# Optimization experiments

Measured on AMD Instinct MI355X. Metric: run time of the kernel, lower is better.

The kernel has to match this reference:

```python
import jax, jax.numpy as jnp
import numpy as np
from jax.scipy.linalg import solve_triangular

LS = 0.5414            # frozen GP length scale (_gp_scale.data = 0.5414)
L2 = LS * LS
D = 2
K_OPS = D + 2          # operators: identity, d/dx_i (i=1..d), laplacian
JITTER_KXX = 1e-5
JITTER_AKA = 1e-4
JITTER_YY = 1e-5


def _opiK(xout, xin, l2, d):
    # op_i applied to first arg of RBF kernel -> (bs, k, m, n)
    r = xout[:, :, None, :] - xin[:, None, :, :]            # (bs,m,n,d)
    u = jnp.sum(r * r, axis=-1) / l2                        # (bs,m,n)
    K = jnp.exp(-0.5 * u)
    ri = jnp.moveaxis(r, -1, 1)                             # (bs,d,m,n)
    grad = -(ri / l2) * K[:, None]                          # d/dx_i K
    lap = ((u - d) / l2) * K                                # Lap_x K
    return jnp.concatenate([K[:, None], grad, lap[:, None]], axis=1)


def _opiKopjfull(x, l2, d):
    # op_i on first arg, op_j on second arg -> (bs, k, k, m, m)
    r = x[:, :, None, :] - x[:, None, :, :]
    u = jnp.sum(r * r, axis=-1) / l2
    K = jnp.exp(-0.5 * u)
    ri = jnp.moveaxis(r, -1, 1)                             # (bs,d,m,m)
    gK = (ri / l2) * K[:, None]                             # d/dy_j K
    lapK = ((u - d) / l2) * K                               # Lap K (either arg)
    eye = jnp.eye(d, dtype=x.dtype)[None, :, :, None, None]
    gg = (eye / l2 - ri[:, :, None] * ri[:, None] / (l2 * l2)) * K[:, None, None]  # d/dx_i d/dy_j K
    glap = (ri / (l2 * l2)) * (((2.0 + d - u) * K)[:, None])  # d/dx_i Lap_y K
    laplap = (((u - d) ** 2 - 4.0 * u + 2.0 * d) / (l2 * l2)) * K  # Lap_x Lap_y K
    row0 = jnp.concatenate([K[:, None, None], gK[:, None], lapK[:, None, None]], axis=2)
    rowg = jnp.concatenate([(-gK)[:, :, None], gg, glap[:, :, None]], axis=2)
    rowl = jnp.concatenate([lapK[:, None, None], (-glap)[:, None], laplap[:, None, None]], axis=2)
    return jnp.concatenate([row0, rowg, rowl], axis=1)


def _psd_solve(L, B):
    # (Kxx + jitter I)^{-1} B via Cholesky (stands in for gpytorch inv_matmul/CG)
    y = solve_triangular(L, B, lower=True)
    return solve_triangular(L, y, lower=True, trans=1)


def _forward(xin, meanin, Kin, weight, bias):
    bs, n, c = meanin.shape
    d, k, l2 = D, K_OPS, L2
    xout, m = xin, n
    r = xin[:, :, None, :] - xin[:, None, :, :]
    Kxx = jnp.exp(-0.5 * jnp.sum(r * r, axis=-1) / l2)      # (bs,n,n)
    In = jnp.eye(n, dtype=xin.dtype)
    Lc = jnp.linalg.cholesky(Kxx + JITTER_KXX * In)
    opiKmn = _opiK(xout, xin, l2, d)                        # (bs,k,m,n)
    # posterior mean of op_i applied to the GP
    opimean = (opiKmn.reshape(bs, k * m, n) @ _psd_solve(Lc, meanin)).reshape(bs, k, m, c)
    Amean = jnp.transpose(opimean, (0, 2, 3, 1)).reshape(bs, m, c * k) @ weight.T + bias
    W = weight.reshape(-1, c, k)                            # (cout,c,k)
    W2 = jnp.einsum('oci,ocj->ij', W, W) / W.shape[0]       # (k,k)
    Kxxinvopi = jnp.swapaxes(
        _psd_solve(Lc, jnp.swapaxes(opiKmn.reshape(bs, k * m, n), 1, 2)), 1, 2)  # (bs,km,n)
    interp_weights = jnp.swapaxes(_psd_solve(Lc, Kin), 1, 2)                      # (bs,n,n)
    opi_interp = jnp.transpose((Kxxinvopi @ interp_weights).reshape(bs, k, m, n), (0, 2, 3, 1))  # (bs,m,n,k)
    Ak_interp = (opi_interp @ W2).reshape(bs, m, n * k)
    Im = jnp.eye(m, dtype=xin.dtype)
    AkinA = Ak_interp @ jnp.transpose(opiKmn, (0, 3, 1, 2)).reshape(bs, n * k, m) + JITTER_AKA * Im
    opiKxxxopj = jnp.transpose(
        (Kxxinvopi @ jnp.swapaxes(opiKmn.reshape(bs, k * m, n), 1, 2)).reshape(bs, k, m, k, m),
        (0, 1, 3, 2, 4))                                    # (bs,k,k,m,m)
    ijkyy = _opiKopjfull(xout, l2, d) - opiKxxxopj          # posterior cov of op_i f, op_j f
    AkAyy = jnp.einsum('bijmp,ij->bmp', ijkyy, W2) + JITTER_YY * Im
    full_AKA = AkinA + AkAyy
    return (xout, Amean, full_AKA)


def setup_inputs() -> dict:
    bs, n, cin, cout = 4, 576, 32, 64
    key = jax.random.key(0)
    k1, k2, k3, k4, k5 = jax.random.split(key, 5)
    xin = jax.random.uniform(k1, (bs, n, D), dtype=jnp.float32) * 6.0
    meanin = jax.random.normal(k2, (bs, n, cin), dtype=jnp.float32)
    A = jax.random.normal(k3, (bs, n, n), dtype=jnp.float32) / np.float32(np.sqrt(n))
    Kin = A @ jnp.swapaxes(A, 1, 2) + 0.1 * jnp.eye(n, dtype=jnp.float32)  # PSD covariance
    fan_in = cin * K_OPS
    weight = jax.random.normal(k4, (cout, fan_in), dtype=jnp.float32) / np.float32(np.sqrt(fan_in))
    bias = jax.random.normal(k5, (cout,), dtype=jnp.float32) * 0.01
    return {"xin": xin, "meanin": meanin, "Kin": Kin, "weight": weight, "bias": bias}


def reference(xin, meanin, Kin, weight, bias):
    return _forward(xin, meanin, Kin, weight, bias)
```

## Files before the change

kernel.cpp:

```cpp
#include <hip/hip_runtime.h>
#include <math.h>

#define NPTS 576
#define N2 331776
#define BSZ 4
#define NB 64
#define NT 9

#define INVL2 (1.0f/0.29311396f)

typedef __attribute__((ext_vector_type(8))) short short8v;
typedef __attribute__((ext_vector_type(16))) float f32x16;

__global__ void copy_xout(const float* __restrict__ xin, float* __restrict__ out) {
    int idx = blockIdx.x * 256 + threadIdx.x;
    out[idx] = xin[idx];
}

__global__ void build_k(const float* __restrict__ xin,
                        float* __restrict__ Kxx, float* __restrict__ opiK) {
    int idx = blockIdx.x * 256 + threadIdx.x;
    int b = idx / N2;
    int rem = idx - b * N2;
    int m = rem / NPTS;
    int nn = rem - m * NPTS;
    const float* xb = xin + (size_t)b * NPTS * 2;
    float xm0 = xb[m*2],  xm1 = xb[m*2+1];
    float xn0 = xb[nn*2], xn1 = xb[nn*2+1];
    float r0 = xm0 - xn0, r1 = xm1 - xn1;
    float u = (r0*r0 + r1*r1) * INVL2;
    float Kv = expf(-0.5f * u);
    Kxx[idx] = Kv + ((m == nn) ? 1e-5f : 0.0f);
    size_t base = (size_t)b * 4 * N2 + rem;
    opiK[base]          = Kv;
    opiK[base + N2]     = -r0 * INVL2 * Kv;
    opiK[base + 2*N2]   = -r1 * INVL2 * Kv;
    opiK[base + 3*N2]   = (u - 2.0f) * INVL2 * Kv;
}

__global__ void w2_k(const float* __restrict__ w, float* __restrict__ W2) {
    __shared__ float red[256];
    int tid = threadIdx.x;
    int pair = tid & 15;
    int slice = tid >> 4;
    int i = pair >> 2, j = pair & 3;
    float s = 0.0f;
    for (int o = slice * 4; o < slice * 4 + 4; ++o)
        for (int c = 0; c < 32; ++c)
            s += w[o*128 + c*4 + i] * w[o*128 + c*4 + j];
    red[tid] = s;
    __syncthreads();
    if (tid < 16) {
        float t = 0.0f;
        #pragma unroll
        for (int k = 0; k < 16; ++k) t += red[pair + 16*k];
        W2[pair] = t * (1.0f/64.0f);
    }
}

__device__ void factor_invert_64(float (*T)[NB+1], float (*V)[NB+1],
                                 float (*tmp)[17], int tid) {
    for (int p = 0; p < 4; ++p) {
        int cp = p * 16;
        if (tid < 64) {
            int r = tid;
            float reg[16];
            #pragma unroll
            for (int q = 0; q < 16; ++q) reg[q] = T[r][cp + q];
            #pragma unroll
            for (int j = 0; j < 16; ++j) {
                int col = cp + j;
                float d2 = __shfl(reg[j], col);
                float d = sqrtf(fmaxf(d2, 1e-12f));
                float lr = (r == col) ? d : reg[j] / d;
                reg[j] = lr;
                #pragma unroll
                for (int q = j + 1; q < 16; ++q) {
                    float lc = __shfl(lr, cp + q);
                    if (r >= cp + q) reg[q] -= lr * lc;
                }
            }
            #pragma unroll
            for (int q = 0; q < 16; ++q) T[r][cp + q] = reg[q];
        }
        __syncthreads();
        int tr = 48 - cp;
        if (tr > 0) {
            for (int idx = tid; idx < tr * tr; idx += 256) {
                int r = cp + 16 + idx / tr;
                int c = cp + 16 + idx % tr;
                if (c <= r) {
                    float s = 0.0f;
                    #pragma unroll
                    for (int k = 0; k < 16; ++k) s += T[r][cp+k] * T[c][cp+k];
                    T[r][c] -= s;
                }
            }
        }
        __syncthreads();
    }
    if (tid < 64) {
        int I = tid >> 4, c = tid & 15, base = I * 16;
        float tcol[16];
        #pragma unroll
        for (int i = 0; i < 16; ++i) tcol[i] = T[base + i][base + c];
        float v[16];
        #pragma unroll
        for (int i = 0; i < 16; ++i) {
            float s = (i == c) ? 1.0f : 0.0f;
            #pragma unroll
            for (int k = 0; k < 16; ++k) {
                if (k < i) {
                    float tik = __shfl(tcol[i], base + k);
                    s -= tik * v[k];
                }
            }
            float tii = __shfl(tcol[i], base + i);
            v[i] = s / tii;
        }
        #pragma unroll
        for (int i = 0; i < 16; ++i) V[base + i][base + c] = v[i];
    }
    __syncthreads();
    const int PI[6] = {1,2,3,2,3,3};
    const int PJ[6] = {0,1,2,0,1,0};
    int rr16 = tid >> 4, cc16 = tid & 15;
    for (int p = 0; p < 6; ++p) {
        int I = PI[p], J = PJ[p];
        float s = 0.0f;
        for (int K = J; K < I; ++K)
            #pragma unroll
            for (int t = 0; t < 16; ++t)
                s += T[I*16+rr16][K*16+t] * V[K*16+t][J*16+cc16];
        tmp[rr16][cc16] = s;
        __syncthreads();
        float s2 = 0.0f;
        for (int t = 0; t <= rr16; ++t) s2 += V[I*16+rr16][I*16+t] * tmp[t][cc16];
        __syncthreads();
        V[I*16+rr16][J*16+cc16] = -s2;
        __syncthreads();
    }
}

__global__ void chol_diag0(const float* __restrict__ A, float* __restrict__ LinvKK) {
    int b = blockIdx.x;
    const float* Ab = A + (size_t)b * N2;
    __shared__ float T[NB][NB+1];
    __shared__ float V[NB][NB+1];
    __shared__ float tmp[16][17];
    int tid = threadIdx.x;
    for (int idx = tid; idx < NB*NB; idx += 256) {
        int r = idx >> 6, c = idx & 63;
        T[r][c] = Ab[(size_t)r * NPTS + c];
        V[r][c] = 0.0f;
    }
    __syncthreads();
    factor_invert_64(T, V, tmp, tid);
    float* Vg = LinvKK + (size_t)b * NT * NB * NB;
    for (int idx = tid; idx < NB*NB; idx += 256) Vg[idx] = V[idx >> 6][idx & 63];
}

__global__ __launch_bounds__(256)
void chol_step(float* __restrict__ A, float* __restrict__ LL,
               float* __restrict__ LinvKK, int kb) {
    int b = blockIdx.y;
    int p = blockIdx.x;
    int ir = 0;
    while (p >= ir + 1) { p -= ir + 1; ir++; }
    int ib = kb + 1 + ir, jb = kb + 1 + p;
    float* Ab = A + (size_t)b * N2;
    float* LLb = LL + (size_t)b * N2;
    __shared__ float Ai[NB][NB+1];
    __shared__ float Aj[NB][NB+1];
    __shared__ float Vs[NB][NB+1];
    __shared__ float tmp[16][17];
    int tid = threadIdx.x;
    int tx = tid & 15, ty = tid >> 4;
    const float* Vg = LinvKK + ((size_t)b * NT + kb) * NB * NB;
    bool diag = (ib == jb);
    for (int idx = tid; idx < NB*NB; idx += 256) {
        int r = idx >> 6, c = idx & 63;
        Ai[r][c] = Ab[(size_t)(ib*NB + r) * NPTS + kb*NB + c];
        Aj[r][c] = diag ? 0.0f : Ab[(size_t)(jb*NB + r) * NPTS + kb*NB + c];
        Vs[r][c] = Vg[idx];
    }
    float U[4][4];
    #pragma unroll
    for (int i = 0; i < 4; ++i)
        #pragma unroll
        for (int j = 0; j < 4; ++j)
            U[i][j] = Ab[(size_t)(ib*NB + ty*4+i) * NPTS + jb*NB + tx*4+j];
    __syncthreads();
    float Li[4][4] = {}, Lj[4][4] = {};
    for (int k = 0; k < NB; ++k) {
        float a[4], v[4];
        #pragma unroll
        for (int i = 0; i < 4; ++i) a[i] = Ai[ty*4+i][k];
        #pragma unroll
        for (int j = 0; j < 4; ++j) v[j] = Vs[tx*4+j][k];
        #pragma unroll
        for (int i = 0; i < 4; ++i)
            #pragma unroll
            for (int j = 0; j < 4; ++j) Li[i][j] += a[i] * v[j];
        if (!diag) {
            float aj[4];
            #pragma unroll
            for (int i = 0; i < 4; ++i) aj[i] = Aj[ty*4+i][k];
            #pragma unroll
            for (int i = 0; i < 4; ++i)
                #pragma unroll
                for (int j = 0; j < 4; ++j) Lj[i][j] += aj[i] * v[j];
        }
    }
    __syncthreads();
    #pragma unroll
    for (int i = 0; i < 4; ++i)
        #pragma unroll
        for (int j = 0; j < 4; ++j) {
            Ai[ty*4+i][tx*4+j] = Li[i][j];
            Aj[ty*4+i][tx*4+j] = diag ? Li[i][j] : Lj[i][j];
        }
    if (diag) {
        #pragma unroll
        for (int i = 0; i < 4; ++i)
            #pragma unroll
            for (int j = 0; j < 4; ++j)
                LLb[(size_t)(ib*NB + ty*4+i) * NPTS + kb*NB + tx*4+j] = Li[i][j];
    }
    __syncthreads();
    float s[4][4] = {};
    for (int k = 0; k < NB; ++k) {
        float a[4], v[4];
        #pragma unroll
        for (int i = 0; i < 4; ++i) a[i] = Ai[ty*4+i][k];
        #pragma unroll
        for (int j = 0; j < 4; ++j) v[j] = Aj[tx*4+j][k];
        #pragma unroll
        for (int i = 0; i < 4; ++i)
            #pragma unroll
            for (int j = 0; j < 4; ++j) s[i][j] += a[i] * v[j];
    }
    #pragma unroll
    for (int i = 0; i < 4; ++i)
        #pragma unroll
        for (int j = 0; j < 4; ++j) U[i][j] -= s[i][j];
    if (blockIdx.x != 0) {
        #pragma unroll
        for (int i = 0; i < 4; ++i)
            #pragma unroll
            for (int j = 0; j < 4; ++j)
                Ab[(size_t)(ib*NB + ty*4+i) * NPTS + jb*NB + tx*4+j] = U[i][j];
        return;
    }
    __syncthreads();
    #pragma unroll
    for (int i = 0; i < 4; ++i)
        #pragma unroll
        for (int j = 0; j < 4; ++j) Ai[ty*4+i][tx*4+j] = U[i][j];
    for (int idx = tid; idx < NB*NB; idx += 256) Aj[idx >> 6][idx & 63] = 0.0f;
    __syncthreads();
    factor_invert_64(Ai, Aj, tmp, tid);
    float* Vo = LinvKK + ((size_t)b * NT + (kb + 1)) * NB * NB;
    for (int idx = tid; idx < NB*NB; idx += 256) Vo[idx] = Aj[idx >> 6][idx & 63];
}

__global__ __launch_bounds__(256)
void trinv_blk(const float* __restrict__ L, const float* __restrict__ LinvKK,
               float* __restrict__ Linv) {
    int sp = blockIdx.x, jb = blockIdx.y, b = blockIdx.z;
    const float* Lb = L + (size_t)b * N2;
    float* Xg = Linv + (size_t)b * N2;
    const float* Vg = LinvKK + (size_t)b * NT * NB * NB;
    int c0 = jb * NB + sp * 16;

    __shared__ float LsT[64][72];
    __shared__ float Xc[576][17];
    __shared__ float Ss[64][17];

    int tid = threadIdx.x;
    int tx = tid & 15, ty = tid >> 4;

    {
        const float* Vjj = Vg + (size_t)jb * NB * NB;
        int r = tid >> 2, c4 = (tid & 3) * 4;
        float4 v = *(const float4*)(Vjj + r * NB + sp * 16 + c4);
        Xc[r][c4+0] = v.x; Xc[r][c4+1] = v.y; Xc[r][c4+2] = v.z; Xc[r][c4+3] = v.w;
        *(float4*)(Xg + (size_t)(jb * NB + r) * NPTS + c0 + c4) = v;
    }
    __syncthreads();

    for (int ib = jb + 1; ib < NT; ++ib) {
        float acc[4] = {};
        for (int kb = jb; kb < ib; ++kb) {
            {
                int r = tid >> 2, t0 = (tid & 3) * 16;
                const float* src = Lb + (size_t)(ib * NB + r) * NPTS + kb * NB + t0;
                #pragma unroll
                for (int q = 0; q < 4; ++q) {
                    float4 v = *(const float4*)(src + q * 4);
                    LsT[t0 + q*4 + 0][r] = v.x;
                    LsT[t0 + q*4 + 1][r] = v.y;
                    LsT[t0 + q*4 + 2][r] = v.z;
                    LsT[t0 + q*4 + 3][r] = v.w;
                }
            }
            __syncthreads();
            int xbase = (kb - jb) * 64;
            #pragma unroll 8
            for (int t = 0; t < 64; ++t) {
                float a4[4]; *(float4*)a4 = *(const float4*)&LsT[t][ty*4];
                float xv = Xc[xbase + t][tx];
                #pragma unroll
                for (int i = 0; i < 4; ++i) acc[i] += a4[i] * xv;
            }
            __syncthreads();
        }
        #pragma unroll
        for (int i = 0; i < 4; ++i) Ss[ty*4+i][tx] = acc[i];
        {
            const float* Vii = Vg + (size_t)ib * NB * NB;
            int r = tid >> 2, t0 = (tid & 3) * 16;
            #pragma unroll
            for (int q = 0; q < 4; ++q) {
                float4 v = *(const float4*)(Vii + r * NB + t0 + q * 4);
                LsT[t0 + q*4 + 0][r] = v.x;
                LsT[t0 + q*4 + 1][r] = v.y;
                LsT[t0 + q*4 + 2][r] = v.z;
                LsT[t0 + q*4 + 3][r] = v.w;
            }
        }
        __syncthreads();
        float acc2[4] = {};
        #pragma unroll 8
        for (int t = 0; t < 64; ++t) {
            float a4[4]; *(float4*)a4 = *(const float4*)&LsT[t][ty*4];
            float sv = Ss[t][tx];
            #pragma unroll
            for (int i = 0; i < 4; ++i) acc2[i] += a4[i] * sv;
        }
        int obase = (ib - jb) * 64;
        #pragma unroll
        for (int i = 0; i < 4; ++i) {
            float v = -acc2[i];
            Xc[obase + ty*4 + i][tx] = v;
            Xg[(size_t)(ib * NB + ty*4 + i) * NPTS + c0 + tx] = v;
        }
        __syncthreads();
    }
}

__device__ inline void split3(float v, unsigned short& h0, unsigned short& h1,
                              unsigned short& h2) {
    unsigned u0 = __float_as_uint(v) & 0xffff0000u;
    float f0 = __uint_as_float(u0);
    float r1 = v - f0;
    unsigned u1 = __float_as_uint(r1) & 0xffff0000u;
    float f1 = __uint_as_float(u1);
    float r2 = r1 - f1;
    h0 = (unsigned short)(u0 >> 16);
    h1 = (unsigned short)(u1 >> 16);
    h2 = (unsigned short)((__float_as_uint(r2) + 0x8000u) >> 16);
}

__device__ inline void pack_store(unsigned short* dst, const unsigned short* v) {
    uint4 w;
    w.x = (unsigned)v[0] | ((unsigned)v[1] << 16);
    w.y = (unsigned)v[2] | ((unsigned)v[3] << 16);
    w.z = (unsigned)v[4] | ((unsigned)v[5] << 16);
    w.w = (unsigned)v[6] | ((unsigned)v[7] << 16);
    *(uint4*)dst = w;
}

template<int EPIB>
__global__ __launch_bounds__(256, 2)
void mm_p2_mfma(const float* __restrict__ Aall, const float* __restrict__ Ball,
                float* __restrict__ Call, long sA, long sB, long sC)
{
    int id = blockIdx.x;
    int x8 = id & 7, qq = id >> 3;
    int nx = qq % 9;
    int band = x8 + 8 * (qq / 9);
    if (band >= 18 * BSZ) return;
    int t  = band % 18;
    int b  = band / 18;
    int pp = t / 9, my = t % 9;
    const float* A0 = Aall + (size_t)b * sA + (size_t)(pp * 2) * N2;
    const float* A1 = A0 + N2;
    const float* B  = Ball + (size_t)b * sB;
    float* C0 = Call + (size_t)b * sC + (size_t)(pp * 2) * N2;
    float* C1 = C0 + N2;
    int n0 = nx * 64, m0 = my * 64;

    __shared__ __align__(16) unsigned short As[12][2][64][8];
    __shared__ __align__(16) unsigned short Bs[6][2][64][8];

    int tid  = threadIdx.x;
    int lane = tid & 63;
    int wid  = tid >> 6;
    int wr = wid >> 1, wc = wid & 1;

    f32x16 acc0, acc1;
    #pragma unroll
    for (int i = 0; i < 16; ++i) { acc0[i] = 0.0f; acc1[i] = 0.0f; }

    int ap   = tid >> 7;
    int aq   = tid & 127;
    int ar   = aq >> 1;
    int asub = aq & 1;
    const float* Apl = ap ? A1 : A0;
    int areg = ar >> 5;
    int aln  = ar & 31;

    int bc   = tid & 63;
    int bkg  = tid >> 6;
    int bsub = bkg >> 1;
    int bln  = (bc & 31) + 32 * (bkg & 1);
    int bwc  = bc >> 5;

    float av[16];
    float bv[8];

    auto loadA = [&](int k0) {
        const float* p = Apl + (size_t)(m0 + ar) * 576 + k0 + asub * 16;
        float4 t0 = *(const float4*)(p);
        float4 t1 = *(const float4*)(p + 4);
        float4 t2 = *(const float4*)(p + 8);
        float4 t3 = *(const float4*)(p + 12);
        av[0]=t0.x;  av[1]=t0.y;  av[2]=t0.z;  av[3]=t0.w;
        av[4]=t1.x;  av[5]=t1.y;  av[6]=t1.z;  av[7]=t1.w;
        av[8]=t2.x;  av[9]=t2.y;  av[10]=t2.z; av[11]=t2.w;
        av[12]=t3.x; av[13]=t3.y; av[14]=t3.z; av[15]=t3.w;
    };
    auto loadB = [&](int k0) {
        const float* p = B + (size_t)(k0 + bkg * 8) * 576 + n0 + bc;
        #pragma unroll
        for (int j = 0; j < 8; ++j) {
            float v = p[(size_t)j * 576];
            if (EPIB) { if (k0 + bkg * 8 + j == n0 + bc) v -= 1.0f; }
            bv[j] = v;
        }
    };
    auto storeA = [&]() {
        unsigned short s0[16], s1[16], s2[16];
        #pragma unroll
        for (int j = 0; j < 16; ++j) split3(av[j], s0[j], s1[j], s2[j]);
        #pragma unroll
        for (int h = 0; h < 2; ++h) {
            int ln = aln + 32 * h;
            pack_store(&As[(ap*3 + 0)*2 + areg][asub][ln][0], &s0[8*h]);
            pack_store(&As[(ap*3 + 1)*2 + areg][asub][ln][0], &s1[8*h]);
            pack_store(&As[(ap*3 + 2)*2 + areg][asub][ln][0], &s2[8*h]);
        }
    };
    auto storeB = [&]() {
        unsigned short s0[8], s1[8], s2[8];
        #pragma unroll
        for (int j = 0; j < 8; ++j) split3(bv[j], s0[j], s1[j], s2[j]);
        pack_store(&Bs[0*2 + bwc][bsub][bln][0], s0);
        pack_store(&Bs[1*2 + bwc][bsub][bln][0], s1);
        pack_store(&Bs[2*2 + bwc][bsub][bln][0], s2);
    };

    const short8v* Af = (const short8v*)As;
    const short8v* Bf = (const short8v*)Bs;

    loadA(0); loadB(0);
    for (int k0 = 0; k0 < 576; k0 += 32) {
        storeA(); storeB();
        __syncthreads();
        if (k0 + 32 < 576) { loadA(k0 + 32); loadB(k0 + 32); }
        #pragma unroll
        for (int sub = 0; sub < 2; ++sub) {
            short8v b0 = Bf[((0*2 + wc)*2 + sub)*64 + lane];
            short8v b1 = Bf[((1*2 + wc)*2 + sub)*64 + lane];
            short8v b2 = Bf[((2*2 + wc)*2 + sub)*64 + lane];
            short8v a0 = Af[((0*3 + 0)*2 + wr)*128 + sub*64 + lane];
            short8v a1 = Af[((0*3 + 1)*2 + wr)*128 + sub*64 + lane];
            short8v a2 = Af[((0*3 + 2)*2 + wr)*128 + sub*64 + lane];
            acc0 = __builtin_amdgcn_mfma_f32_32x32x16_bf16(a0, b0, acc0, 0, 0, 0);
            acc0 = __builtin_amdgcn_mfma_f32_32x32x16_bf16(a0, b1, acc0, 0, 0, 0);
            acc0 = __builtin_amdgcn_mfma_f32_32x32x16_bf16(a1, b0, acc0, 0, 0, 0);
            acc0 = __builtin_amdgcn_mfma_f32_32x32x16_bf16(a1, b1, acc0, 0, 0, 0);
            acc0 = __builtin_amdgcn_mfma_f32_32x32x16_bf16(a0, b2, acc0, 0, 0, 0);
            acc0 = __builtin_amdgcn_mfma_f32_32x32x16_bf16(a2, b0, acc0, 0, 0, 0);
            a0 = Af[((1*3 + 0)*2 + wr)*128 + sub*64 + lane];
            a1 = Af[((1*3 + 1)*2 + wr)*128 + sub*64 + lane];
            a2 = Af[((1*3 + 2)*2 + wr)*128 + sub*64 + lane];
            acc1 = __builtin_amdgcn_mfma_f32_32x32x16_bf16(a0, b0, acc1, 0, 0, 0);
            acc1 = __builtin_amdgcn_mfma_f32_32x32x16_bf16(a0, b1, acc1, 0, 0, 0);
            acc1 = __builtin_amdgcn_mfma_f32_32x32x16_bf16(a1, b0, acc1, 0, 0, 0);
            acc1 = __builtin_amdgcn_mfma_f32_32x32x16_bf16(a1, b1, acc1, 0, 0, 0);
            acc1 = __builtin_amdgcn_mfma_f32_32x32x16_bf16(a0, b2, acc1, 0, 0, 0);
            acc1 = __builtin_amdgcn_mfma_f32_32x32x16_bf16(a2, b0, acc1, 0, 0, 0);
        }
        __syncthreads();
    }

    int colg = n0 + 32*wc + (lane & 31);
    int rowb = m0 + 32*wr + 4*(lane >> 5);
    #pragma unroll
    for (int reg = 0; reg < 16; ++reg) {
        int row = rowb + (reg & 3) + 8*(reg >> 2);
        C0[(size_t)row * 576 + colg] = acc0[reg];
        C1[(size_t)row * 576 + colg] = acc1[reg];
    }
}

__global__ __launch_bounds__(256, 2)
void mm_abt_mfma(const float* __restrict__ Aall, const float* __restrict__ Ball,
                 float* __restrict__ Call, long sA, long sB, long sC, long sSplit)
{
    int p = blockIdx.x;
    int ir = 0;
    while (p >= ir + 1) { p -= ir + 1; ir++; }
    int my = ir, nx = p;
    int zz = blockIdx.z;
    int sp = zz & 3, b = zz >> 2;
    const float* A = Aall + (size_t)b * sA + (size_t)sp * N2;
    const float* B = Ball + (size_t)b * sB + (size_t)sp * N2;
    float* Cp = Call + (size_t)b * sC + (size_t)sp * sSplit;
    int m0 = my * 64, n0 = nx * 64;

    __shared__ __align__(16) unsigned short Fr[12][2][64][8];

    int tid  = threadIdx.x;
    int lane = tid & 63;
    int wid  = tid >> 6;
    int wr = wid >> 1, wc = wid & 1;

    f32x16 acc;
    #pragma unroll
    for (int i = 0; i < 16; ++i) acc[i] = 0.0f;

    int sel  = tid >> 7;
    int q2   = tid & 127;
    int r    = q2 >> 1;
    int ssub = q2 & 1;
    const float* Src = sel ? B : A;
    int base0 = sel ? n0 : m0;
    int rreg = r >> 5;
    int rln  = r & 31;

    float av[16];

    auto loadF = [&](int k0) {
        const float* pp = Src + (size_t)(base0 + r) * 576 + k0 + ssub * 16;
        float4 t0 = *(const float4*)(pp);
        float4 t1 = *(const float4*)(pp + 4);
        float4 t2 = *(const float4*)(pp + 8);
        float4 t3 = *(const float4*)(pp + 12);
        av[0]=t0.x;  av[1]=t0.y;  av[2]=t0.z;  av[3]=t0.w;
        av[4]=t1.x;  av[5]=t1.y;  av[6]=t1.z;  av[7]=t1.w;
        av[8]=t2.x;  av[9]=t2.y;  av[10]=t2.z; av[11]=t2.w;
        av[12]=t3.x; av[13]=t3.y; av[14]=t3.z; av[15]=t3.w;
    };
    auto storeF = [&]() {
        unsigned short s0[16], s1[16], s2[16];
        #pragma unroll
        for (int j = 0; j < 16; ++j) split3(av[j], s0[j], s1[j], s2[j]);
        #pragma unroll
        for (int h = 0; h < 2; ++h) {
            int ln = rln + 32 * h;
            pack_store(&Fr[sel*6 + 0*2 + rreg][ssub][ln][0], &s0[8*h]);
            pack_store(&Fr[sel*6 + 1*2 + rreg][ssub][ln][0], &s1[8*h]);
            pack_store(&Fr[sel*6 + 2*2 + rreg][ssub][ln][0], &s2[8*h]);
        }
    };

    const short8v* Ff = (const short8v*)Fr;

    loadF(0);
    for (int k0 = 0; k0 < 576; k0 += 32) {
        storeF();
        __syncthreads();
        if (k0 + 32 < 576) loadF(k0 + 32);
        #pragma unroll
        for (int sub = 0; sub < 2; ++sub) {
            short8v a0 = Ff[((0*2 + wr)*2 + sub)*64 + lane];
            short8v a1 = Ff[((1*2 + wr)*2 + sub)*64 + lane];
            short8v a2 = Ff[((2*2 + wr)*2 + sub)*64 + lane];
            short8v b0 = Ff[((6 + 0*2 + wc)*2 + sub)*64 + lane];
            short8v b1 = Ff[((6 + 1*2 + wc)*2 + sub)*64 + lane];
            short8v b2 = Ff[((6 + 2*2 + wc)*2 + sub)*64 + lane];
            acc = __builtin_amdgcn_mfma_f32_32x32x16_bf16(a0, b0, acc, 0, 0, 0);
            acc = __builtin_amdgcn_mfma_f32_32x32x16_bf16(a0, b1, acc, 0, 0, 0);
            acc = __builtin_amdgcn_mfma_f32_32x32x16_bf16(a1, b0, acc, 0, 0, 0);
            acc = __builtin_amdgcn_mfma_f32_32x32x16_bf16(a1, b1, acc, 0, 0, 0);
            acc = __builtin_amdgcn_mfma_f32_32x32x16_bf16(a0, b2, acc, 0, 0, 0);
            acc = __builtin_amdgcn_mfma_f32_32x32x16_bf16(a2, b0, acc, 0, 0, 0);
        }
        __syncthreads();
    }

    int colg = n0 + 32*wc + (lane & 31);
    int rowb = m0 + 32*wr + 4*(lane >> 5);
    #pragma unroll
    for (int reg = 0; reg < 16; ++reg) {
        int row = rowb + (reg & 3) + 8*(reg >> 2);
        Cp[(size_t)row * 576 + colg] = acc[reg];
    }
}

template<int TA, int TB, int SK, int TRI, int SWZ, int EPIB, int TRIC>
__global__ __launch_bounds__(256)
void mm_kernel(const float* __restrict__ Aall, const float* __restrict__ Ball,
               float* __restrict__ Call,
               int M, int N, int K, int planeK,
               int lda, int ldb, int ldc,
               long sA, long sB, long sC, long pA, long pB, long sSplit, int MT)
{
    int nx, my, zz;
    if (TRIC) {
        int p = blockIdx.x;
        int ir = 0;
        while (p >= ir + 1) { p -= ir + 1; ir++; }
        my = ir; nx = p; zz = blockIdx.z;
    } else if (SWZ) {
        int id = blockIdx.x;
        int x8 = id & 7;
        int q  = id >> 3;
        nx = q % 9;
        int band = x8 + 8 * (q / 9);
        if (band >= MT * 4 * SK) return;
        my = band % MT;
        zz = band / MT;
    } else { nx = blockIdx.x; my = blockIdx.y; zz = blockIdx.z; }
    int sp = (SK > 1) ? (zz % SK) : 0;
    int b  = (SK > 1) ? (zz / SK) : zz;
    const float* A = Aall + (size_t)b * sA;
    const float* B = Ball + (size_t)b * sB;
    float* C = Call + (size_t)b * sC + (size_t)sp * sSplit;
    int n0 = nx * 64;
    int m0 = my * 64;

    __shared__ float As[16][68];
    __shared__ float Bs[16][68];

    int tid = threadIdx.x;
    int tx = tid & 15, ty = tid >> 4;

    float acc[4][4] = {};
    bool mFull = (m0 + 64 <= M);
    bool nFull = (n0 + 64 <= N);

    int triBeg = 0;
    if (TRI) { int mx = (m0 > n0 ? m0 : n0); triBeg = mx & ~15; }
    int kBeg = triBeg, kEnd = K;
    if (SK > 1) {
        int len = K - triBeg;
        int chunk = ((len / SK) + 15) & ~15;
        kBeg = triBeg + sp * chunk;
        if (kBeg > K) kBeg = K;
        kEnd = (sp == SK - 1) ? K : (kBeg + chunk < K ? kBeg + chunk : K);
    }

    float avr[4];
    float bvr[4];

    auto loadA = [&](int k0) {
        int plane = k0 / planeK;
        int koff  = k0 - plane * planeK;
        if (TA == 0) {
            const float* Ab = A + (size_t)pA * plane;
            int r = tid >> 2, c4 = (tid & 3) * 4;
            int gm = m0 + r;
            if (mFull || gm < M) {
                float4 t = *(const float4*)(Ab + (size_t)gm * lda + koff + c4);
                avr[0]=t.x; avr[1]=t.y; avr[2]=t.z; avr[3]=t.w;
            } else { avr[0]=avr[1]=avr[2]=avr[3]=0.0f; }
        } else {
            int r = tid >> 4, c4 = (tid & 15) * 4;
            const float* p = A + (size_t)(koff + r) * lda + m0 + c4;
            if (mFull) {
                float4 t = *(const float4*)p;
                avr[0]=t.x; avr[1]=t.y; avr[2]=t.z; avr[3]=t.w;
            } else {
                #pragma unroll
                for (int jj = 0; jj < 4; ++jj)
                    avr[jj] = (m0 + c4 + jj < M) ? p[jj] : 0.0f;
            }
        }
    };
    auto storeA = [&]() {
        if (TA == 0) {
            int r = tid >> 2, c4 = (tid & 3) * 4;
            #pragma unroll
            for (int q = 0; q < 4; ++q) As[c4+q][r] = avr[q];
        } else {
            int r = tid >> 4, c4 = (tid & 15) * 4;
            #pragma unroll
            for (int q = 0; q < 4; ++q) As[r][c4+q] = avr[q];
        }
    };
    auto loadB = [&](int k0) {
        int plane = k0 / planeK;
        int koff  = k0 - plane * planeK;
        if (TB == 0) {
            int r = tid >> 4, c4 = (tid & 15) * 4;
            const float* p = B + (size_t)(koff + r) * ldb + n0 + c4;
            if (nFull) {
                float4 t = *(const float4*)p;
                bvr[0]=t.x; bvr[1]=t.y; bvr[2]=t.z; bvr[3]=t.w;
            } else {
                #pragma unroll
                for (int jj = 0; jj < 4; ++jj)
                    bvr[jj] = (n0 + c4 + jj < N) ? p[jj] : 0.0f;
            }
            if (EPIB) {
                int gk = koff + r;
                #pragma unroll
                for (int jj = 0; jj < 4; ++jj)
                    if (gk == n0 + c4 + jj) bvr[jj] -= 1.0f;
            }
        } else {
            const float* Bb = B + (size_t)pB * plane;
            int r = tid >> 2, c4 = (tid & 3) * 4;
            int gp = n0 + r;
            if (nFull || gp < N) {
                float4 t = *(const float4*)(Bb + (size_t)gp * ldb + koff + c4);
                bvr[0]=t.x; bvr[1]=t.y; bvr[2]=t.z; bvr[3]=t.w;
            } else { bvr[0]=bvr[1]=bvr[2]=bvr[3]=0.0f; }
        }
    };
    auto storeB = [&]() {
        if (TB == 0) {
            int r = tid >> 4, c4 = (tid & 15) * 4;
            #pragma unroll
            for (int q = 0; q < 4; ++q) Bs[r][c4+q] = bvr[q];
        } else {
            int r = tid >> 2, c4 = (tid & 3) * 4;
            #pragma unroll
            for (int q = 0; q < 4; ++q) Bs[c4+q][r] = bvr[q];
        }
    };

    if (kBeg < kEnd) {
        loadA(kBeg); loadB(kBeg);
        for (int k0 = kBeg; k0 < kEnd; k0 += 16) {
            storeA(); storeB();
            __syncthreads();
            if (k0 + 16 < kEnd) { loadA(k0 + 16); loadB(k0 + 16); }
            #pragma unroll
            for (int kk = 0; kk < 16; ++kk) {
                float a[4], bb[4];
                *(float4*)a  = *(const float4*)&As[kk][ty*4];
                *(float4*)bb = *(const float4*)&Bs[kk][tx*4];
                #pragma unroll
                for (int i = 0; i < 4; ++i)
                    #pragma unroll
                    for (int j = 0; j < 4; ++j)
                        acc[i][j] += a[i] * bb[j];
            }
            __syncthreads();
        }
    }

    #pragma unroll
    for (int i = 0; i < 4; ++i) {
        int gm = m0 + ty*4 + i;
        if (gm >= M) continue;
        #pragma unroll
        for (int j = 0; j < 4; ++j) {
            int gn = n0 + tx*4 + j;
            if (gn >= N) continue;
            C[(size_t)gm * ldc + gn] = acc[i][j];
        }
    }
}

__global__ void combine_add2(const float* __restrict__ p0, float* __restrict__ o,
                             long stride) {
    int i = blockIdx.x * 256 + threadIdx.x;
    float4 x = ((const float4*)p0)[i];
    float4 y = ((const float4*)(p0 + stride))[i];
    float4 r; r.x=x.x+y.x; r.y=x.y+y.y; r.z=x.z+y.z; r.w=x.w+y.w;
    ((float4*)o)[i] = r;
}

__global__ void combine_solm4(const float* __restrict__ p, float* __restrict__ o) {
    int i = blockIdx.x * 256 + threadIdx.x;
    o[i] = p[i] + p[i + 73728] + p[i + 2*73728] + p[i + 3*73728];
}

__global__ void combine_prior4_sym(const float* __restrict__ p0,
                                   const float* __restrict__ xin,
                                   const float* __restrict__ W2g,
                                   float* __restrict__ o, long stride) {
    __shared__ float w[16];
    int tid = threadIdx.x;
    if (tid < 16) w[tid] = W2g[tid];
    __syncthreads();
    int idx = blockIdx.x * 256 + tid;
    int b = idx / N2;
    int rem = idx - b * N2;
    int m = rem / NPTS, n = rem - m * NPTS;
    if (m < n) return;
    const float* xb = xin + (size_t)b * NPTS * 2;
    float r0 = xb[m*2+0] - xb[n*2+0];
    float r1 = xb[m*2+1] - xb[n*2+1];
    float u = (r0*r0 + r1*r1) * INVL2;
    float Kv = expf(-0.5f * u);
    float i2 = INVL2 * INVL2;
    float gK0 = r0 * INVL2 * Kv;
    float gK1 = r1 * INVL2 * Kv;
    float lapK = (u - 2.0f) * INVL2 * Kv;
    float gg00 = (INVL2 - r0*r0*i2) * Kv;
    float gg01 = (-r0*r1*i2) * Kv;
    float gg11 = (INVL2 - r1*r1*i2) * Kv;
    float gl0 = r0 * i2 * (4.0f - u) * Kv;
    float gl1 = r1 * i2 * (4.0f - u) * Kv;
    float ll = ((u-2.0f)*(u-2.0f) - 4.0f*u + 4.0f) * i2 * Kv;
    float prior =
          w[0]*Kv + w[1]*gK0 + w[2]*gK1 + w[3]*lapK
        + w[4]*(-gK0) + w[5]*gg00 + w[6]*gg01 + w[7]*gl0
        + w[8]*(-gK1) + w[9]*gg01 + w[10]*gg11 + w[11]*gl1
        + w[12]*lapK + w[13]*(-gl0) + w[14]*(-gl1) + w[15]*ll;
    float v = p0[idx] + p0[idx + stride] + p0[idx + 2*stride] + p0[idx + 3*stride]
            + prior;
    if (m == n) v += 1.1e-4f;
    o[(size_t)b * N2 + (size_t)m * NPTS + n] = v;
    if (m != n)
        o[(size_t)b * N2 + (size_t)n * NPTS + m] = v;
}

__global__ void opiw2_k(const float* __restrict__ opiK, const float* __restrict__ W2,
                        float* __restrict__ outB) {
    int idx = blockIdx.x * 256 + threadIdx.x;
    int b = idx / N2;
    int rem = idx - b * N2;
    size_t base = (size_t)b * 4 * N2 + rem;
    float k0 = opiK[base], k1 = opiK[base + N2], k2 = opiK[base + 2*N2], k3 = opiK[base + 3*N2];
    #pragma unroll
    for (int i = 0; i < 4; ++i)
        outB[base + (size_t)i * N2] = W2[i*4+0]*k0 + W2[i*4+1]*k1 + W2[i*4+2]*k2 + W2[i*4+3]*k3;
}

__global__ __launch_bounds__(256)
void amean_k(const float* __restrict__ opimean, const float* __restrict__ weight,
             const float* __restrict__ bias, float* __restrict__ out) {
    int b = blockIdx.y;
    int m0 = blockIdx.x * 32;
    __shared__ float Wl[64][128];
    __shared__ float om[32][128];
    int tid = threadIdx.x;
    for (int idx = tid; idx < 64*128; idx += 256) Wl[idx / 128][idx & 127] = weight[idx];
    for (int idx = tid; idx < 32*128; idx += 256) {
        int m = idx >> 7, ck = idx & 127, c = ck >> 2, kop = ck & 3;
        om[m][ck] = opimean[((size_t)b * 4 + kop) * NPTS * 32 + (size_t)(m0 + m) * 32 + c];
    }
    __syncthreads();
    int ml = tid >> 3, o0 = (tid & 7) * 8;
    float acc[8] = {};
    for (int ck = 0; ck < 128; ++ck) {
        float v = om[ml][ck];
        #pragma unroll
        for (int q = 0; q < 8; ++q) acc[q] += v * Wl[o0+q][ck];
    }
    #pragma unroll
    for (int q = 0; q < 8; ++q)
        out[4608 + ((size_t)b * NPTS + m0 + ml) * 64 + o0 + q] = acc[q] + bias[o0+q];
}

static inline int gridSwz(int MT, int Z) { return 8 * 9 * ((MT * Z + 7) / 8); }

extern "C" void kernel_launch(void* const* d_in, const int* in_sizes, int n_in,
                              void* d_out, int out_size, void* d_ws, size_t ws_size,
                              hipStream_t stream) {
    const float* xin    = (const float*)d_in[0];
    const float* meanin = (const float*)d_in[1];
    const float* Kin    = (const float*)d_in[2];
    const float* weight = (const float*)d_in[3];
    const float* bias   = (const float*)d_in[4];
    float* out = (float*)d_out;
    float* ws  = (float*)d_ws;

    const long N2L = N2;
    float* W2      = ws;
    float* LinvKK  = ws + 64;
    float* R1 = LinvKK + 147456;
    float* R2 = R1 + 4*N2L;
    float* R3 = R2 + 4*N2L;
    float* R4 = R3 + 4*N2L;
    float* R5 = R4 + 16*N2L;
    float* R6 = R5 + 16*N2L;

    hipMemsetAsync(R2, 0, (size_t)4 * N2 * sizeof(float), stream);
    copy_xout<<<dim3(18), dim3(256), 0, stream>>>(xin, out);
    build_k<<<dim3((BSZ*N2)/256), dim3(256), 0, stream>>>(xin, R1, R4);
    w2_k<<<dim3(1), dim3(256), 0, stream>>>(weight, W2);
    chol_diag0<<<dim3(BSZ), dim3(256), 0, stream>>>(R1, LinvKK);
    for (int kb = 0; kb < NT - 1; ++kb) {
        int t = NT - 1 - kb;
        chol_step<<<dim3(t*(t+1)/2, BSZ), dim3(256), 0, stream>>>(R1, R3, LinvKK, kb);
    }
    trinv_blk<<<dim3(4, NT, BSZ), dim3(256), 0, stream>>>(R3, LinvKK, R2);
    mm_kernel<1,0,2,1,1,0,0><<<dim3(gridSwz(9,8)), dim3(256), 0, stream>>>(
        R2, R2, R5, 576,576,576,576, 576,576,576,
        N2L,N2L,N2L, 0,0, 4*N2L, 9);
    combine_add2<<<dim3(1296), dim3(256), 0, stream>>>(R5, R3, 4*N2L);
    mm_kernel<0,0,4,0,0,0,0><<<dim3(1,9,16), dim3(256), 0, stream>>>(
        R3, meanin, R6, 576,32,576,576, 576,32,32,
        N2L,18432,18432, 0,0, 73728, 9);
    combine_solm4<<<dim3(288), dim3(256), 0, stream>>>(R6, R2);
    mm_kernel<0,0,1,0,0,0,0><<<dim3(1,36,BSZ), dim3(256), 0, stream>>>(
        R4, R2, R2 + 73728, 2304,32,576,576, 576,32,32,
        4*N2L,18432,73728, 0,0, 0, 9);
    amean_k<<<dim3(18,BSZ), dim3(256), 0, stream>>>(R2 + 73728, weight, bias, out);
    mm_kernel<0,0,2,0,1,0,0><<<dim3(gridSwz(9,8)), dim3(256), 0, stream>>>(
        Kin, R3, R6, 576,576,576,576, 576,576,576,
        N2L,N2L,N2L, 0,0, 4*N2L, 9);
    combine_add2<<<dim3(1296), dim3(256), 0, stream>>>(R6, R1, 4*N2L);
    mm_p2_mfma<0><<<dim3(gridSwz(18,4)), dim3(256), 0, stream>>>(
        R4, R3, R5, 4*N2L, N2L, 4*N2L);
    opiw2_k<<<dim3((BSZ*N2)/256), dim3(256), 0, stream>>>(R4, W2, R4);
    mm_p2_mfma<1><<<dim3(gridSwz(18,4)), dim3(256), 0, stream>>>(
        R5, R1, R6, 4*N2L, N2L, 4*N2L);
    mm_abt_mfma<<<dim3(45,1,BSZ*4), dim3(256), 0, stream>>>(
        R6, R4, R5, 4*N2L, 4*N2L, N2L, 4*N2L);
    combine_prior4_sym<<<dim3(5184), dim3(256), 0, stream>>>(
        R5, xin, W2, out + 152064, 4*N2L);
}
```

Baseline: 906.0 us.

## Replace split-K FP32 GEMMs with bf16x3 MFMA kernels, dropping combine passes

Replaces two split-K scalar FP32 GEMMs and their add-combine kernels with MFMA kernels that use a three-way bf16 split to approximate fp32 accuracy. One computes L^T L for the inverse Cholesky factor. It launches only lower-triangle tiles, starts K at the tile row because the factor is triangular, and mirrors each result into the upper half. The other computes Kin times Kinv directly without split-K. This removes the partial-sum buffers and combine launches, at the cost of fewer blocks per GEMM and a small extra error from the bf16 split.

```diff
diff --git a/kernel.cpp b/kernel.cpp
--- a/kernel.cpp
+++ b/kernel.cpp
@@ -598,6 +598,197 @@
     for (int reg = 0; reg < 16; ++reg) {
         int row = rowb + (reg & 3) + 8*(reg >> 2);
         Cp[(size_t)row * 576 + colg] = acc[reg];
+    }
+}
+
+__global__ __launch_bounds__(256, 2)
+void mm_ata_mfma(const float* __restrict__ Lg, float* __restrict__ C,
+                 long sA, long sC)
+{
+    int p = blockIdx.x;
+    int ir = 0;
+    while (p >= ir + 1) { p -= ir + 1; ir++; }
+    int my = ir, nx = p;
+    int b = blockIdx.z;
+    const float* A = Lg + (size_t)b * sA;
+    float* Cb = C + (size_t)b * sC;
+    int m0 = my * 64, n0 = nx * 64;
+    int kBeg = m0;
+
+    __shared__ __align__(16) unsigned short Fr[12][2][64][8];
+
+    int tid  = threadIdx.x;
+    int lane = tid & 63;
+    int wid  = tid >> 6;
+    int wr = wid >> 1, wc = wid & 1;
+
+    f32x16 acc;
+    #pragma unroll
+    for (int i = 0; i < 16; ++i) acc[i] = 0.0f;
+
+    int sel  = tid >> 7;
+    int q2   = tid & 127;
+    int col  = q2 & 63;
+    int ssub = q2 >> 6;
+    int c0base = sel ? n0 : m0;
+    int rreg = col >> 5;
+    int rln  = col & 31;
+
+    float av[16];
+
+    auto loadF = [&](int k0) {
+        const float* pp = A + (size_t)(k0 + ssub * 16) * 576 + c0base + col;
+        #pragma unroll
+        for (int j = 0; j < 16; ++j) av[j] = pp[(size_t)j * 576];
+    };
+    auto storeF = [&]() {
+        unsigned short s0[16], s1[16], s2[16];
+        #pragma unroll
+        for (int j = 0; j < 16; ++j) split3(av[j], s0[j], s1[j], s2[j]);
+        #pragma unroll
+        for (int h = 0; h < 2; ++h) {
+            int ln = rln + 32 * h;
+            pack_store(&Fr[sel*6 + 0*2 + rreg][ssub][ln][0], &s0[8*h]);
+            pack_store(&Fr[sel*6 + 1*2 + rreg][ssub][ln][0], &s1[8*h]);
+            pack_store(&Fr[sel*6 + 2*2 + rreg][ssub][ln][0], &s2[8*h]);
+        }
+    };
+
+    const short8v* Ff = (const short8v*)Fr;
+
+    loadF(kBeg);
+    for (int k0 = kBeg; k0 < 576; k0 += 32) {
+        storeF();
+        __syncthreads();
+        if (k0 + 32 < 576) loadF(k0 + 32);
+        #pragma unroll
+        for (int sub = 0; sub < 2; ++sub) {
+            short8v a0 = Ff[((0*2 + wr)*2 + sub)*64 + lane];
+            short8v a1 = Ff[((1*2 + wr)*2 + sub)*64 + lane];
+            short8v a2 = Ff[((2*2 + wr)*2 + sub)*64 + lane];
+            short8v b0 = Ff[((6 + 0*2 + wc)*2 + sub)*64 + lane];
+            short8v b1 = Ff[((6 + 1*2 + wc)*2 + sub)*64 + lane];
+            short8v b2 = Ff[((6 + 2*2 + wc)*2 + sub)*64 + lane];
+            acc = __builtin_amdgcn_mfma_f32_32x32x16_bf16(a0, b0, acc, 0, 0, 0);
+            acc = __builtin_amdgcn_mfma_f32_32x32x16_bf16(a0, b1, acc, 0, 0, 0);
+            acc = __builtin_amdgcn_mfma_f32_32x32x16_bf16(a1, b0, acc, 0, 0, 0);
+            acc = __builtin_amdgcn_mfma_f32_32x32x16_bf16(a1, b1, acc, 0, 0, 0);
+            acc = __builtin_amdgcn_mfma_f32_32x32x16_bf16(a0, b2, acc, 0, 0, 0);
+            acc = __builtin_amdgcn_mfma_f32_32x32x16_bf16(a2, b0, acc, 0, 0, 0);
+        }
+        __syncthreads();
+    }
+
+    int colg = n0 + 32*wc + (lane & 31);
+    int rowb = m0 + 32*wr + 4*(lane >> 5);
+    #pragma unroll
+    for (int reg = 0; reg < 16; ++reg) {
+        int row = rowb + (reg & 3) + 8*(reg >> 2);
+        float v = acc[reg];
+        Cb[(size_t)row * 576 + colg] = v;
+        Cb[(size_t)colg * 576 + row] = v;
+    }
+}
+
+__global__ __launch_bounds__(256, 2)
+void mm_ab_mfma(const float* __restrict__ Aall, const float* __restrict__ Ball,
+                float* __restrict__ Call, long sA, long sB, long sC)
+{
+    int nx = blockIdx.x % 9, my = blockIdx.x / 9;
+    int b = blockIdx.z;
+    const float* A = Aall + (size_t)b * sA;
+    const float* B = Ball + (size_t)b * sB;
+    float* Cb = Call + (size_t)b * sC;
+    int m0 = my * 64, n0 = nx * 64;
+
+    __shared__ __align__(16) unsigned short Fr[12][2][64][8];
+
+    int tid  = threadIdx.x;
+    int lane = tid & 63;
+    int wid  = tid >> 6;
+    int wr = wid >> 1, wc = wid & 1;
+
+    f32x16 acc;
+    #pragma unroll
+    for (int i = 0; i < 16; ++i) acc[i] = 0.0f;
+
+    int sel  = tid >> 7;
+    int q2   = tid & 127;
+    int ar   = q2 >> 1;
+    int asub = q2 & 1;
+    int areg = ar >> 5, aln = ar & 31;
+    int bcol = q2 & 63;
+    int bssub = q2 >> 6;
+    int breg = bcol >> 5, brln = bcol & 31;
+
+    float av[16];
+
+    auto loadF = [&](int k0) {
+        if (sel == 0) {
+            const float* pp = A + (size_t)(m0 + ar) * 576 + k0 + asub * 16;
+            float4 t0 = *(const float4*)(pp);
+            float4 t1 = *(const float4*)(pp + 4);
+            float4 t2 = *(const float4*)(pp + 8);
+            float4 t3 = *(const float4*)(pp + 12);
+            av[0]=t0.x;  av[1]=t0.y;  av[2]=t0.z;  av[3]=t0.w;
+            av[4]=t1.x;  av[5]=t1.y;  av[6]=t1.z;  av[7]=t1.w;
+            av[8]=t2.x;  av[9]=t2.y;  av[10]=t2.z; av[11]=t2.w;
+            av[12]=t3.x; av[13]=t3.y; av[14]=t3.z; av[15]=t3.w;
+        } else {
+            const float* pp = B + (size_t)(k0 + bssub * 16) * 576 + n0 + bcol;
+            #pragma unroll
+            for (int j = 0; j < 16; ++j) av[j] = pp[(size_t)j * 576];
+        }
+    };
+    auto storeF = [&]() {
+        unsigned short s0[16], s1[16], s2[16];
+        #pragma unroll
+        for (int j = 0; j < 16; ++j) split3(av[j], s0[j], s1[j], s2[j]);
+        int reg0 = sel ? (6 + 0*2 + breg) : (0*2 + areg);
+        int reg1 = sel ? (6 + 1*2 + breg) : (1*2 + areg);
+        int reg2 = sel ? (6 + 2*2 + breg) : (2*2 + areg);
+        int sb   = sel ? bssub : asub;
+        int ln0  = sel ? brln : aln;
+        #pragma unroll
+        for (int h = 0; h < 2; ++h) {
+            int ln = ln0 + 32 * h;
+            pack_store(&Fr[reg0][sb][ln][0], &s0[8*h]);
+            pack_store(&Fr[reg1][sb][ln][0], &s1[8*h]);
+            pack_store(&Fr[reg2][sb][ln][0], &s2[8*h]);
+        }
+    };
+
+    const short8v* Ff = (const short8v*)Fr;
+
+    loadF(0);
+    for (int k0 = 0; k0 < 576; k0 += 32) {
+        storeF();
+        __syncthreads();
+        if (k0 + 32 < 576) loadF(k0 + 32);
+        #pragma unroll
+        for (int sub = 0; sub < 2; ++sub) {
+            short8v a0 = Ff[((0*2 + wr)*2 + sub)*64 + lane];
+            short8v a1 = Ff[((1*2 + wr)*2 + sub)*64 + lane];
+            short8v a2 = Ff[((2*2 + wr)*2 + sub)*64 + lane];
+            short8v b0 = Ff[((6 + 0*2 + wc)*2 + sub)*64 + lane];
+            short8v b1 = Ff[((6 + 1*2 + wc)*2 + sub)*64 + lane];
+            short8v b2 = Ff[((6 + 2*2 + wc)*2 + sub)*64 + lane];
+            acc = __builtin_amdgcn_mfma_f32_32x32x16_bf16(a0, b0, acc, 0, 0, 0);
+            acc = __builtin_amdgcn_mfma_f32_32x32x16_bf16(a0, b1, acc, 0, 0, 0);
+            acc = __builtin_amdgcn_mfma_f32_32x32x16_bf16(a1, b0, acc, 0, 0, 0);
+            acc = __builtin_amdgcn_mfma_f32_32x32x16_bf16(a1, b1, acc, 0, 0, 0);
+            acc = __builtin_amdgcn_mfma_f32_32x32x16_bf16(a0, b2, acc, 0, 0, 0);
+            acc = __builtin_amdgcn_mfma_f32_32x32x16_bf16(a2, b0, acc, 0, 0, 0);
+        }
+        __syncthreads();
+    }
+
+    int colg = n0 + 32*wc + (lane & 31);
+    int rowb = m0 + 32*wr + 4*(lane >> 5);
+    #pragma unroll
+    for (int reg = 0; reg < 16; ++reg) {
+        int row = rowb + (reg & 3) + 8*(reg >> 2);
+        Cb[(size_t)row * 576 + colg] = acc[reg];
     }
 }
 
@@ -766,15 +957,6 @@
             C[(size_t)gm * ldc + gn] = acc[i][j];
         }
     }
-}
-
-__global__ void combine_add2(const float* __restrict__ p0, float* __restrict__ o,
-                             long stride) {
-    int i = blockIdx.x * 256 + threadIdx.x;
-    float4 x = ((const float4*)p0)[i];
-    float4 y = ((const float4*)(p0 + stride))[i];
-    float4 r; r.x=x.x+y.x; r.y=x.y+y.y; r.z=x.z+y.z; r.w=x.w+y.w;
-    ((float4*)o)[i] = r;
 }
 
 __global__ void combine_solm4(const float* __restrict__ p, float* __restrict__ o) {
@@ -894,10 +1076,7 @@
         chol_step<<<dim3(t*(t+1)/2, BSZ), dim3(256), 0, stream>>>(R1, R3, LinvKK, kb);
     }
     trinv_blk<<<dim3(4, NT, BSZ), dim3(256), 0, stream>>>(R3, LinvKK, R2);
-    mm_kernel<1,0,2,1,1,0,0><<<dim3(gridSwz(9,8)), dim3(256), 0, stream>>>(
-        R2, R2, R5, 576,576,576,576, 576,576,576,
-        N2L,N2L,N2L, 0,0, 4*N2L, 9);
-    combine_add2<<<dim3(1296), dim3(256), 0, stream>>>(R5, R3, 4*N2L);
+    mm_ata_mfma<<<dim3(45, 1, BSZ), dim3(256), 0, stream>>>(R2, R3, N2L, N2L);
     mm_kernel<0,0,4,0,0,0,0><<<dim3(1,9,16), dim3(256), 0, stream>>>(
         R3, meanin, R6, 576,32,576,576, 576,32,32,
         N2L,18432,18432, 0,0, 73728, 9);
@@ -906,10 +1085,8 @@
         R4, R2, R2 + 73728, 2304,32,576,576, 576,32,32,
         4*N2L,18432,73728, 0,0, 0, 9);
     amean_k<<<dim3(18,BSZ), dim3(256), 0, stream>>>(R2 + 73728, weight, bias, out);
-    mm_kernel<0,0,2,0,1,0,0><<<dim3(gridSwz(9,8)), dim3(256), 0, stream>>>(
-        Kin, R3, R6, 576,576,576,576, 576,576,576,
-        N2L,N2L,N2L, 0,0, 4*N2L, 9);
-    combine_add2<<<dim3(1296), dim3(256), 0, stream>>>(R6, R1, 4*N2L);
+    mm_ab_mfma<<<dim3(81, 1, BSZ), dim3(256), 0, stream>>>(
+        Kin, R3, R1, N2L, N2L, N2L);
     mm_p2_mfma<0><<<dim3(gridSwz(18,4)), dim3(256), 0, stream>>>(
         R4, R3, R5, 4*N2L, N2L, 4*N2L);
     opiw2_k<<<dim3((BSZ*N2)/256), dim3(256), 0, stream>>>(R4, W2, R4);
```

Result: no change. 889.5 us, median of 2 (-1.8%).
